# Performance work log

Measured on AMD Instinct MI355X. Metric: run time of the kernel, lower is better.

The kernel has to match this reference:

```python
import jax, jax.numpy as jnp
import numpy as np

EPS = 1e-6  # torch F.pairwise_distance default eps (added to diff before norm)


def setup_inputs() -> dict:
    key = jax.random.key(0)
    k1, k2 = jax.random.split(key)
    B, D, n = 4096, 1024, 64
    K = n * n
    x = jax.random.normal(k1, (B, D), dtype=jnp.float32)
    weight = jax.random.normal(k2, (D, K), dtype=jnp.float32)  # SOM codebook
    # locations = [(gx, gy) for gx in range(n) for gy in range(n)]
    gx, gy = jnp.meshgrid(jnp.arange(n), jnp.arange(n), indexing='ij')
    locations = jnp.stack([gx, gy], axis=-1).reshape(K, 2).astype(jnp.float32)
    return {"x": x, "weight": weight, "locations": locations}


def _pairwise_l2(x, weight):
    # torch: norm(x[:, :, None] - weight[None] + EPS, p=2, dim=1) -> [B, K]
    # Expanded algebraically to avoid the [B, D, K] intermediate:
    D = x.shape[1]
    x2 = jnp.sum(x * x, axis=1, keepdims=True)            # [B, 1]
    w2 = jnp.sum(weight * weight, axis=0, keepdims=True)  # [1, K]
    xw = x @ weight                                        # [B, K] GEMM
    sx = jnp.sum(x, axis=1, keepdims=True)                 # [B, 1]
    sw = jnp.sum(weight, axis=0, keepdims=True)            # [1, K]
    d2 = x2 - 2.0 * xw + w2 + 2.0 * EPS * (sx - sw) + D * EPS * EPS
    return jnp.sqrt(jnp.maximum(d2, 0.0))


def reference(x, weight, locations):
    B = x.shape[0]
    dists = _pairwise_l2(x, weight)                        # [B, K]
    losses = jnp.min(dists, axis=1, keepdims=True)         # [B, 1]
    bmu_indexes = jnp.argmin(dists, axis=1, keepdims=True)  # [B, 1] int
    bmu_locations = locations[bmu_indexes]                 # [B, 1, 2]
    loss = jnp.sum(losses) / B                             # scalar
    return bmu_locations, loss, bmu_indexes
```

## Files before the change

### kernel.cpp

```cpp
#include <hip/hip_runtime.h>

#define EPS 1e-6f

constexpr int Bn = 4096;
constexpr int Dn = 1024;
constexpr int Kn = 4096;

typedef __attribute__((ext_vector_type(4))) float f32x4;
typedef __attribute__((ext_vector_type(2))) long long ll2;

__device__ inline int pk_fp8_lo(float a, float b, int old) {
    return __builtin_amdgcn_cvt_pk_fp8_f32(a, b, old, false);
}
__device__ inline int pk_fp8_hi(float a, float b, int old) {
    return __builtin_amdgcn_cvt_pk_fp8_f32(a, b, old, true);
}

__device__ inline float packcand(float s, int k) {
    unsigned b = __float_as_uint(fmaxf(s, 0.5f));
    return __uint_as_float((b & 0xFFFFF000u) | (unsigned)k);
}

__global__ __launch_bounds__(256) void som_prep(
    const float* __restrict__ x, const float* __restrict__ w,
    unsigned char* __restrict__ xf8, float* __restrict__ rrow,
    float* __restrict__ wtf, unsigned char* __restrict__ wf8,
    float* __restrict__ cpart) {
    __shared__ float t[64][65];
    __shared__ float cp[4][64];
    __shared__ float red[8];
    const int tid = threadIdx.x;
    const int bid = blockIdx.x;
    if (bid < 2048) {
        const int lane = tid & 63, wid = tid >> 6;
        size_t i = (size_t)bid * 256 + tid;
        const float4* p = (const float4*)x;
        float4 a = p[i * 2], b = p[i * 2 + 1];
        int lo = pk_fp8_lo(a.x, a.y, 0); lo = pk_fp8_hi(a.z, a.w, lo);
        int hi = pk_fp8_lo(b.x, b.y, 0); hi = pk_fp8_hi(b.z, b.w, hi);
        ((int2*)xf8)[i] = make_int2(lo, hi);
        float s2 = a.x*a.x + a.y*a.y + a.z*a.z + a.w*a.w
                 + b.x*b.x + b.y*b.y + b.z*b.z + b.w*b.w;
        float s1 = a.x + a.y + a.z + a.w + b.x + b.y + b.z + b.w;
        #pragma unroll
        for (int off = 1; off < 64; off <<= 1) {
            s2 += __shfl_xor(s2, off);
            s1 += __shfl_xor(s1, off);
        }
        if (lane == 0) { red[wid] = s2; red[4 + wid] = s1; }
        __syncthreads();
        if (tid == 0)
            rrow[bid * 2] = (red[0] + red[1])
                + 2.f * EPS * (red[4] + red[5]) + (float)Dn * EPS * EPS;
        if (tid == 128)
            rrow[bid * 2 + 1] = (red[2] + red[3])
                + 2.f * EPS * (red[6] + red[7]) + (float)Dn * EPS * EPS;
    } else {
        const int tb = bid - 2048;
        const int kb = tb & 63, db = tb >> 6;
        const int k0 = kb * 64, d0 = db * 64;
        const int l16 = tid & 15, g16 = tid >> 4;
        #pragma unroll
        for (int i = 0; i < 4; ++i) {
            int r = i * 16 + g16;
            float4 v = *(const float4*)&w[(size_t)(d0 + r) * Kn + k0 + l16 * 4];
            t[r][l16 * 4 + 0] = v.x; t[r][l16 * 4 + 1] = v.y;
            t[r][l16 * 4 + 2] = v.z; t[r][l16 * 4 + 3] = v.w;
        }
        __syncthreads();
        #pragma unroll
        for (int i = 0; i < 4; ++i) {
            int kr = i * 16 + g16;
            float4 v;
            v.x = t[l16 * 4 + 0][kr]; v.y = t[l16 * 4 + 1][kr];
            v.z = t[l16 * 4 + 2][kr]; v.w = t[l16 * 4 + 3][kr];
            *(float4*)&wtf[(size_t)(k0 + kr) * Dn + d0 + l16 * 4] = v;
            int pk = pk_fp8_lo(v.x, v.y, 0); pk = pk_fp8_hi(v.z, v.w, pk);
            *(unsigned int*)&wf8[(size_t)(k0 + kr) * Dn + d0 + l16 * 4] =
                (unsigned int)pk;
        }
        const int tx = tid & 63, ty = tid >> 6;
        float cs = 0.f;
        #pragma unroll
        for (int j = 0; j < 16; ++j) {
            float v = t[ty * 16 + j][tx];
            cs = fmaf(v, v - 2.f * EPS, cs);
        }
        cp[ty][tx] = cs;
        __syncthreads();
        if (ty == 0)
            cpart[(size_t)db * Kn + k0 + tx] = cp[0][tx] + cp[1][tx] + cp[2][tx] + cp[3][tx];
    }
}

__global__ __launch_bounds__(256, 3) void som_gemm_fp8(
    const unsigned char* __restrict__ xf8, const unsigned char* __restrict__ wf8,
    const float* __restrict__ cpart, float* __restrict__ pval) {
    __shared__ __align__(16) unsigned char As[128 * 144];
    __shared__ __align__(16) unsigned char Bs[128 * 144];
    const int tid = threadIdx.x;
    const int lane = tid & 63;
    const int wid = tid >> 6;
    const int wm = wid >> 1, wn = wid & 1;
    const int f = blockIdx.x;
    const int xcd = f & 7;
    const int ib = f >> 3;
    const int rb = xcd * 4 + (ib & 3);
    const int cb = ib >> 2;
    const int rowBase = rb * 128, colBase = cb * 128;

    int offA[4];
    const unsigned char* gsrcA[4];
    const unsigned char* gsrcB[4];
    #pragma unroll
    for (int i = 0; i < 4; ++i) {
        int g = i * 256 + tid;
        int r = g >> 3, s = g & 7;
        offA[i] = r * 144 + (2 * (s & 1)) * 32 + (s >> 1) * 8;
        gsrcA[i] = xf8 + (size_t)(rowBase + r) * Dn + s * 16;
        gsrcB[i] = wf8 + (size_t)(colBase + r) * Dn + s * 16;
    }

    f32x4 acc[4][4] = {};
    ll2 ra[4], rbv[4];
    #pragma unroll
    for (int i = 0; i < 4; ++i) {
        ra[i]  = *(const ll2*)(gsrcA[i]);
        rbv[i] = *(const ll2*)(gsrcB[i]);
    }

    const int mrA = (wm * 64 + (lane & 15)) * 144;
    const int nrB = (wn * 64 + (lane & 15)) * 144;
    const int qoff = (lane >> 4) * 32;

    for (int it = 0; it < 8; ++it) {
        #pragma unroll
        for (int i = 0; i < 4; ++i) {
            *(long long*)&As[offA[i]]      = ra[i][0];
            *(long long*)&As[offA[i] + 32] = ra[i][1];
            *(long long*)&Bs[offA[i]]      = rbv[i][0];
            *(long long*)&Bs[offA[i] + 32] = rbv[i][1];
        }
        __syncthreads();
        if (it < 7) {
            int d0 = (it + 1) * 128;
            #pragma unroll
            for (int i = 0; i < 4; ++i) {
                ra[i]  = *(const ll2*)(gsrcA[i] + d0);
                rbv[i] = *(const ll2*)(gsrcB[i] + d0);
            }
        }
        #pragma unroll
        for (int kk2 = 0; kk2 < 2; ++kk2) {
            ll2 a2[4], b2[4];
            #pragma unroll
            for (int i = 0; i < 4; ++i) {
                a2[i] = *(const ll2*)&As[mrA + i * 16 * 144 + qoff + kk2 * 16];
                b2[i] = *(const ll2*)&Bs[nrB + i * 16 * 144 + qoff + kk2 * 16];
            }
            #pragma unroll
            for (int i = 0; i < 4; ++i)
                #pragma unroll
                for (int j = 0; j < 4; ++j) {
                    acc[i][j] = __builtin_amdgcn_mfma_f32_16x16x32_fp8_fp8(
                        a2[i][0], b2[j][0], acc[i][j], 0, 0, 0);
                    acc[i][j] = __builtin_amdgcn_mfma_f32_16x16x32_fp8_fp8(
                        a2[i][1], b2[j][1], acc[i][j], 0, 0, 0);
                }
        }
        __syncthreads();
    }

    const int cn = lane & 15, q = lane >> 4;
    const int nbase = colBase + wn * 64;
    float cv[4];
    #pragma unroll
    for (int j = 0; j < 4; ++j) {
        float s = 0.f;
        #pragma unroll
        for (int db = 0; db < 16; ++db)
            s += cpart[(size_t)db * Kn + nbase + j * 16 + cn];
        cv[j] = s;
    }
    #pragma unroll
    for (int i = 0; i < 4; ++i) {
        #pragma unroll
        for (int rg = 0; rg < 4; ++rg) {
            float p1 = 3.4e38f, p2 = 3.4e38f;
            #pragma unroll
            for (int j = 0; j < 4; ++j) {
                float p = packcand(fmaf(-2.f, acc[i][j][rg], cv[j]),
                                   nbase + j * 16 + cn);
                float lo = fminf(p1, p), hi = fmaxf(p1, p);
                p1 = lo; p2 = fminf(p2, hi);
            }
            #pragma unroll
            for (int off = 1; off < 16; off <<= 1) {
                float o1 = __shfl_xor(p1, off);
                float o2 = __shfl_xor(p2, off);
                float lo = fminf(p1, o1), hi = fmaxf(p1, o1);
                p1 = lo; p2 = fminf(hi, fminf(p2, o2));
            }
            if (cn == 0) {
                int mrow = rowBase + wm * 64 + i * 16 + q * 4 + rg;
                size_t e = (size_t)mrow * 128 + cb * 4 + wn * 2;
                pval[e] = p1; pval[e + 1] = p2;
            }
        }
    }
}

__global__ __launch_bounds__(256) void som_finalize(
    const float* __restrict__ x, const float* __restrict__ wtf,
    const float* __restrict__ cpart, const float* __restrict__ loc,
    const float* __restrict__ pval, const float* __restrict__ rrow,
    float* __restrict__ dist, float* __restrict__ out) {
    const int lane = threadIdx.x & 63;
    const int row = blockIdx.x * 4 + (threadIdx.x >> 6);

    const float4* xr = (const float4*)(x + (size_t)row * Dn);
    float4 xv[4];
    #pragma unroll
    for (int j = 0; j < 4; ++j) xv[j] = xr[lane * 4 + j];
    const float rrv = rrow[row];

    float v0 = pval[(size_t)row * 128 + lane];
    float v1 = pval[(size_t)row * 128 + 64 + lane];
    float g = fminf(v0, v1);
    #pragma unroll
    for (int off = 1; off < 64; off <<= 1) g = fminf(g, __shfl_xor(g, off));
    const float thr = g + 30.0f;
    unsigned long long m0 = __ballot(v0 <= thr);
    unsigned long long m1 = __ballot(v1 <= thr);

    float bestd2 = 3.4e38f; int bestk = 0x7fffffff;
    #pragma unroll
    for (int slot = 0; slot < 2; ++slot) {
        unsigned long long m = slot ? m1 : m0;
        float vs = slot ? v1 : v0;
        while (m) {
            int src = __builtin_ctzll(m); m &= m - 1;
            int k = ((int)__float_as_uint(__shfl(vs, src))) & 0xFFF;
            const float4* wr = (const float4*)(wtf + (size_t)k * Dn);
            float pa = (lane < 16) ? cpart[(size_t)lane * Kn + k] : 0.f;
            float da = 0.f;
            #pragma unroll
            for (int j = 0; j < 4; ++j) {
                float4 wv = wr[lane * 4 + j];
                da += xv[j].x * wv.x + xv[j].y * wv.y + xv[j].z * wv.z + xv[j].w * wv.w;
            }
            pa -= 2.f * da;
            #pragma unroll
            for (int off = 1; off < 64; off <<= 1) pa += __shfl_xor(pa, off);
            float d2 = rrv + pa;
            if (d2 < bestd2 || (d2 == bestd2 && k < bestk)) { bestd2 = d2; bestk = k; }
        }
    }
    if (lane == 0) {
        out[2 * row]     = loc[2 * bestk];
        out[2 * row + 1] = loc[2 * bestk + 1];
        out[8193 + row]  = (float)bestk;
        dist[row]        = sqrtf(fmaxf(bestd2, 0.f));
    }
}

__global__ __launch_bounds__(256) void som_loss(const float* __restrict__ dist,
                                                float* __restrict__ out) {
    __shared__ float red[4];
    const int tid = threadIdx.x;
    const int lane = tid & 63, wid = tid >> 6;
    const float4* p = (const float4*)dist;
    float s = 0.f;
    #pragma unroll
    for (int j = 0; j < 4; ++j) {
        float4 v = p[tid + j * 256];
        s += v.x + v.y + v.z + v.w;
    }
    #pragma unroll
    for (int off = 1; off < 64; off <<= 1) s += __shfl_xor(s, off);
    if (lane == 0) red[wid] = s;
    __syncthreads();
    if (tid == 0)
        out[8192] = (red[0] + red[1] + red[2] + red[3]) * (1.0f / (float)Bn);
}

extern "C" void kernel_launch(void* const* d_in, const int* in_sizes, int n_in,
                              void* d_out, int out_size, void* d_ws, size_t ws_size,
                              hipStream_t stream) {
    const float* x   = (const float*)d_in[0];
    const float* w   = (const float*)d_in[1];
    const float* loc = (const float*)d_in[2];
    float* out = (float*)d_out;

    float* rrow = (float*)d_ws;
    float* wtf  = rrow + Bn;
    unsigned char* wf8 = (unsigned char*)(wtf + (size_t)Kn * Dn);
    unsigned char* xf8 = wf8 + (size_t)Kn * Dn;
    float* pval = (float*)(xf8 + (size_t)Bn * Dn);
    float* cpart = pval + (size_t)Bn * 128;
    float* dist  = cpart + 16 * Kn;

    som_prep<<<3072, 256, 0, stream>>>(x, w, xf8, rrow, wtf, wf8, cpart);
    som_gemm_fp8<<<1024, 256, 0, stream>>>(xf8, wf8, cpart, pval);
    som_finalize<<<Bn / 4, 256, 0, stream>>>(x, wtf, cpart, loc, pval, rrow, dist, out);
    som_loss<<<1, 256, 0, stream>>>(dist, out);
}
```

Before: 136.5 us.

## Use 16x16x128 fp8 MFMA with direct global-to-LDS loads and swizzled layout

Replaces the 16x16x32 fp8 MFMA pairs with the gfx950 16x16x128 f8f6f4 MFMA via inline asm. Global fp8 operands are now written by the prep kernel in a permuted, XOR-swizzled column order, so the GEMM can use global_load_lds to copy 16-byte chunks straight into unpadded LDS without a register staging pass. The goal is fewer MFMA issues, less VGPR traffic and fewer LDS bank conflicts. The cost is that it depends on exact layout agreement between prep and GEMM, and on the asm MFMA and async LDS loads being ordered correctly by the barriers alone, with no explicit wait on the LDS loads.

```diff
diff --git a/kernel.cpp b/kernel.cpp
--- a/kernel.cpp
+++ b/kernel.cpp
@@ -7,7 +7,8 @@
 constexpr int Kn = 4096;
 
 typedef __attribute__((ext_vector_type(4))) float f32x4;
-typedef __attribute__((ext_vector_type(2))) long long ll2;
+typedef __attribute__((ext_vector_type(4))) int   i32x4;
+typedef __attribute__((ext_vector_type(8))) int   i32x8;
 
 __device__ inline int pk_fp8_lo(float a, float b, int old) {
     return __builtin_amdgcn_cvt_pk_fp8_f32(a, b, old, false);
@@ -19,6 +20,18 @@
 __device__ inline float packcand(float s, int k) {
     unsigned b = __float_as_uint(fmaxf(s, 0.5f));
     return __uint_as_float((b & 0xFFFFF000u) | (unsigned)k);
+}
+
+__device__ inline int permoff(int dc, int r) {
+    int db = dc & 127;
+    int pcol = ((db >> 3) & 3) * 32 + ((db >> 5) & 3) * 8 + (db & 7);
+    return (dc & ~127) + (pcol ^ ((r & 7) << 4));
+}
+
+__device__ inline void gload16(const unsigned char* g, unsigned char* l) {
+    __builtin_amdgcn_global_load_lds(
+        (const __attribute__((address_space(1))) void*)g,
+        (__attribute__((address_space(3))) void*)l, 16, 0, 0);
 }
 
 __global__ __launch_bounds__(256) void som_prep(
@@ -34,11 +47,13 @@
     if (bid < 2048) {
         const int lane = tid & 63, wid = tid >> 6;
         size_t i = (size_t)bid * 256 + tid;
+        const int row = (int)(i >> 7);
+        const int d0 = (int)(i & 127) * 8;
         const float4* p = (const float4*)x;
         float4 a = p[i * 2], b = p[i * 2 + 1];
         int lo = pk_fp8_lo(a.x, a.y, 0); lo = pk_fp8_hi(a.z, a.w, lo);
         int hi = pk_fp8_lo(b.x, b.y, 0); hi = pk_fp8_hi(b.z, b.w, hi);
-        ((int2*)xf8)[i] = make_int2(lo, hi);
+        *(int2*)(xf8 + (size_t)row * Dn + permoff(d0, row)) = make_int2(lo, hi);
         float s2 = a.x*a.x + a.y*a.y + a.z*a.z + a.w*a.w
                  + b.x*b.x + b.y*b.y + b.z*b.z + b.w*b.w;
         float s1 = a.x + a.y + a.z + a.w + b.x + b.y + b.z + b.w;
@@ -76,7 +91,8 @@
             v.z = t[l16 * 4 + 2][kr]; v.w = t[l16 * 4 + 3][kr];
             *(float4*)&wtf[(size_t)(k0 + kr) * Dn + d0 + l16 * 4] = v;
             int pk = pk_fp8_lo(v.x, v.y, 0); pk = pk_fp8_hi(v.z, v.w, pk);
-            *(unsigned int*)&wf8[(size_t)(k0 + kr) * Dn + d0 + l16 * 4] =
+            const int krow = k0 + kr;
+            *(unsigned int*)&wf8[(size_t)krow * Dn + permoff(d0 + l16 * 4, krow)] =
                 (unsigned int)pk;
         }
         const int tx = tid & 63, ty = tid >> 6;
@@ -93,11 +109,11 @@
     }
 }
 
-__global__ __launch_bounds__(256, 3) void som_gemm_fp8(
+__global__ __launch_bounds__(256, 3) void som_gemm_mx(
     const unsigned char* __restrict__ xf8, const unsigned char* __restrict__ wf8,
     const float* __restrict__ cpart, float* __restrict__ pval) {
-    __shared__ __align__(16) unsigned char As[128 * 144];
-    __shared__ __align__(16) unsigned char Bs[128 * 144];
+    __shared__ __align__(16) unsigned char As[128 * 128];
+    __shared__ __align__(16) unsigned char Bs[128 * 128];
     const int tid = threadIdx.x;
     const int lane = tid & 63;
     const int wid = tid >> 6;
@@ -109,66 +125,53 @@
     const int cb = ib >> 2;
     const int rowBase = rb * 128, colBase = cb * 128;
 
-    int offA[4];
-    const unsigned char* gsrcA[4];
-    const unsigned char* gsrcB[4];
+    const unsigned char* gA0 = xf8 + (size_t)(rowBase + wid * 8 + (lane >> 3)) * Dn + (lane & 7) * 16;
+    const unsigned char* gB0 = wf8 + (size_t)(colBase + wid * 8 + (lane >> 3)) * Dn + (lane & 7) * 16;
+    unsigned char* lA0 = &As[(wid * 8) * 128];
+    unsigned char* lB0 = &Bs[(wid * 8) * 128];
+
+    f32x4 acc[4][4] = {};
+
+    const int arow = wm * 64 + (lane & 15);
+    const int brow = wn * 64 + (lane & 15);
+    const int q32 = (lane >> 4) * 32;
+    const int aL = q32 ^ ((arow & 7) << 4), aH = (q32 + 16) ^ ((arow & 7) << 4);
+    const int bL = q32 ^ ((brow & 7) << 4), bH = (q32 + 16) ^ ((brow & 7) << 4);
+
     #pragma unroll
     for (int i = 0; i < 4; ++i) {
-        int g = i * 256 + tid;
-        int r = g >> 3, s = g & 7;
-        offA[i] = r * 144 + (2 * (s & 1)) * 32 + (s >> 1) * 8;
-        gsrcA[i] = xf8 + (size_t)(rowBase + r) * Dn + s * 16;
-        gsrcB[i] = wf8 + (size_t)(colBase + r) * Dn + s * 16;
-    }
-
-    f32x4 acc[4][4] = {};
-    ll2 ra[4], rbv[4];
-    #pragma unroll
-    for (int i = 0; i < 4; ++i) {
-        ra[i]  = *(const ll2*)(gsrcA[i]);
-        rbv[i] = *(const ll2*)(gsrcB[i]);
-    }
-
-    const int mrA = (wm * 64 + (lane & 15)) * 144;
-    const int nrB = (wn * 64 + (lane & 15)) * 144;
-    const int qoff = (lane >> 4) * 32;
+        gload16(gA0 + (size_t)i * 32 * Dn, lA0 + i * 32 * 128);
+        gload16(gB0 + (size_t)i * 32 * Dn, lB0 + i * 32 * 128);
+    }
 
     for (int it = 0; it < 8; ++it) {
+        __syncthreads();
+        i32x8 af[4];
         #pragma unroll
         for (int i = 0; i < 4; ++i) {
-            *(long long*)&As[offA[i]]      = ra[i][0];
-            *(long long*)&As[offA[i] + 32] = ra[i][1];
-            *(long long*)&Bs[offA[i]]      = rbv[i][0];
-            *(long long*)&Bs[offA[i] + 32] = rbv[i][1];
+            i32x4 lo = *(const i32x4*)&As[(arow + i * 16) * 128 + aL];
+            i32x4 hi = *(const i32x4*)&As[(arow + i * 16) * 128 + aH];
+            af[i] = __builtin_shufflevector(lo, hi, 0, 1, 2, 3, 4, 5, 6, 7);
+        }
+        #pragma unroll
+        for (int j = 0; j < 4; ++j) {
+            i32x4 lo = *(const i32x4*)&Bs[(brow + j * 16) * 128 + bL];
+            i32x4 hi = *(const i32x4*)&Bs[(brow + j * 16) * 128 + bH];
+            i32x8 bf = __builtin_shufflevector(lo, hi, 0, 1, 2, 3, 4, 5, 6, 7);
+            #pragma unroll
+            for (int i = 0; i < 4; ++i)
+                asm("v_mfma_f32_16x16x128_f8f6f4 %0, %1, %2, %0"
+                    : "+v"(acc[i][j]) : "v"(af[i]), "v"(bf));
         }
         __syncthreads();
         if (it < 7) {
-            int d0 = (it + 1) * 128;
+            const int d0n = (it + 1) * 128;
             #pragma unroll
             for (int i = 0; i < 4; ++i) {
-                ra[i]  = *(const ll2*)(gsrcA[i] + d0);
-                rbv[i] = *(const ll2*)(gsrcB[i] + d0);
-            }
-        }
-        #pragma unroll
-        for (int kk2 = 0; kk2 < 2; ++kk2) {
-            ll2 a2[4], b2[4];
-            #pragma unroll
-            for (int i = 0; i < 4; ++i) {
-                a2[i] = *(const ll2*)&As[mrA + i * 16 * 144 + qoff + kk2 * 16];
-                b2[i] = *(const ll2*)&Bs[nrB + i * 16 * 144 + qoff + kk2 * 16];
-            }
-            #pragma unroll
-            for (int i = 0; i < 4; ++i)
-                #pragma unroll
-                for (int j = 0; j < 4; ++j) {
-                    acc[i][j] = __builtin_amdgcn_mfma_f32_16x16x32_fp8_fp8(
-                        a2[i][0], b2[j][0], acc[i][j], 0, 0, 0);
-                    acc[i][j] = __builtin_amdgcn_mfma_f32_16x16x32_fp8_fp8(
-                        a2[i][1], b2[j][1], acc[i][j], 0, 0, 0);
-                }
-        }
-        __syncthreads();
+                gload16(gA0 + (size_t)i * 32 * Dn + d0n, lA0 + i * 32 * 128);
+                gload16(gB0 + (size_t)i * 32 * Dn + d0n, lB0 + i * 32 * 128);
+            }
+        }
     }
 
     const int cn = lane & 15, q = lane >> 4;
@@ -301,7 +304,7 @@
     float* dist  = cpart + 16 * Kn;
 
     som_prep<<<3072, 256, 0, stream>>>(x, w, xf8, rrow, wtf, wf8, cpart);
-    som_gemm_fp8<<<1024, 256, 0, stream>>>(xf8, wf8, cpart, pval);
+    som_gemm_mx<<<1024, 256, 0, stream>>>(xf8, wf8, cpart, pval);
     som_finalize<<<Bn / 4, 256, 0, stream>>>(x, wtf, cpart, loc, pval, rrow, dist, out);
     som_loss<<<1, 256, 0, stream>>>(dist, out);
 }
```

Measured after the change: 136.1 us. About the same (-0.3%).
